# Performance work log

Hardware: AMD Instinct MI355X
Metric: run time of the kernel (lower is better)

The kernel has to match this reference:

```python
import jax, jax.numpy as jnp
import numpy as np


def setup_inputs() -> dict:
    key = jax.random.key(0)
    k0, k1 = jax.random.split(key)
    b, n, m, e = 8, 2048, 2048, 1024
    mat_0 = jax.random.normal(k0, (b, n, e), dtype=jnp.float32)
    mat_1 = jax.random.normal(k1, (b, m, e), dtype=jnp.float32)
    return {"mat_0": mat_0, "mat_1": mat_1}


def reference(mat_0, mat_1):
    # Original tiles to [b,n,m,e], multiplies, and sums over e.
    # Mathematically identical to a batched QK^T matmul: [b,n,m].
    return jnp.einsum('bne,bme->bnm', mat_0, mat_1)
```

## Files before the change

### kernel.cpp

```cpp
#include <hip/hip_runtime.h>
#include <hip/hip_bf16.h>

typedef __attribute__((ext_vector_type(8))) short short8;
typedef __attribute__((ext_vector_type(4))) float f32x4;
typedef __attribute__((ext_vector_type(4))) unsigned int u32x4;
typedef unsigned short u16;
typedef __attribute__((address_space(1))) void gvoid;
typedef __attribute__((address_space(3))) void lvoid;

static constexpr int BATCH = 8;
static constexpr int NDIM  = 2048;
static constexpr int MDIM  = 2048;
static constexpr int EDIM  = 1024;
static constexpr int BM    = 128;
static constexpr int BN    = 128;
static constexpr int BK    = 32;
static constexpr int KIT   = EDIM / BK;

__device__ __forceinline__ unsigned bf16rne_pair(float a, float b) {
  unsigned ua = __float_as_uint(a), ub = __float_as_uint(b);
  ua = (ua + 0x7FFFu + ((ua >> 16) & 1u)) >> 16;
  ub = (ub + 0x7FFFu + ((ub >> 16) & 1u)) >> 16;
  return ua | (ub << 16);
}

__global__ __launch_bounds__(256)
void cvt_kernel(const float* __restrict__ A, const float* __restrict__ B,
                u16* __restrict__ Abf, u16* __restrict__ Bbf) {
  const int half = (BATCH * NDIM * EDIM) / (256 * 8);
  int bid = blockIdx.x;
  const float* src; u16* dst;
  if (bid < half) { src = A; dst = Abf; }
  else            { src = B; dst = Bbf; bid -= half; }
  size_t idx = ((size_t)bid * 256 + threadIdx.x) * 8;
  f32x4 x = *(const f32x4*)(src + idx);
  f32x4 y = *(const f32x4*)(src + idx + 4);
  u32x4 r;
  r[0] = bf16rne_pair(x[0], x[1]);
  r[1] = bf16rne_pair(x[2], x[3]);
  r[2] = bf16rne_pair(y[0], y[1]);
  r[3] = bf16rne_pair(y[2], y[3]);
  *(u32x4*)(dst + idx) = r;
}

__device__ __forceinline__ void async_cp16(const void* g, void* l) {
  __builtin_amdgcn_global_load_lds((gvoid*)g, (lvoid*)l, 16, 0, 0);
}

__global__ __launch_bounds__(256, 3)
void bmm_bf16_kernel(const u16* __restrict__ A, const u16* __restrict__ B,
                     float* __restrict__ C) {
  __shared__ u16 As[BM * BK];
  __shared__ u16 Bs[BN * BK];

  const int tid  = threadIdx.x;
  const int lane = tid & 63;
  const int wave = tid >> 6;
  const int quad = lane >> 4;
  const int ml   = lane & 15;
  const int wrow = (wave >> 1) * 64;
  const int wcol = (wave & 1) * 64;

  const int tcol  = blockIdx.x;
  const int trow  = blockIdx.y;
  const int batch = blockIdx.z;

  const u16* Ab = A + (size_t)batch * NDIM * EDIM + (size_t)trow * BM * EDIM;
  const u16* Bb = B + (size_t)batch * MDIM * EDIM + (size_t)tcol * BN * EDIM;
  float*     Cb = C + (size_t)batch * NDIM * MDIM;

  const int rA0 = wave * 16;
  const int rA1 = wave * 16 + 64;
  const int lrow = lane >> 2;
  const int lcol = (lane & 3) * 8;

  const u16* gA0 = Ab + (size_t)(rA0 + lrow) * EDIM + lcol;
  const u16* gA1 = Ab + (size_t)(rA1 + lrow) * EDIM + lcol;
  const u16* gB0 = Bb + (size_t)(rA0 + lrow) * EDIM + lcol;
  const u16* gB1 = Bb + (size_t)(rA1 + lrow) * EDIM + lcol;
  u16* lA0 = &As[rA0 * BK];
  u16* lA1 = &As[rA1 * BK];
  u16* lB0 = &Bs[rA0 * BK];
  u16* lB1 = &Bs[rA1 * BK];

  f32x4 acc[4][4] = {};

  for (int kb = 0; kb < KIT; ++kb) {
    const int ko = kb * BK;
    __syncthreads();
    async_cp16(gA0 + ko, lA0);
    async_cp16(gA1 + ko, lA1);
    async_cp16(gB0 + ko, lB0);
    async_cp16(gB1 + ko, lB1);
    __syncthreads();

    short8 af[4], bfr[4];
#pragma unroll
    for (int i = 0; i < 4; ++i)
      af[i] = *(const short8*)&As[(wrow + i * 16 + ml) * BK + quad * 8];
#pragma unroll
    for (int i = 0; i < 4; ++i)
      bfr[i] = *(const short8*)&Bs[(wcol + i * 16 + ml) * BK + quad * 8];

#pragma unroll
    for (int mi = 0; mi < 4; ++mi)
#pragma unroll
      for (int ni = 0; ni < 4; ++ni)
        acc[mi][ni] = __builtin_amdgcn_mfma_f32_16x16x32_bf16(
            af[mi], bfr[ni], acc[mi][ni], 0, 0, 0);
  }

  const int crow = trow * BM + wrow + quad * 4;
  const int ccol = tcol * BN + wcol + ml;
#pragma unroll
  for (int mi = 0; mi < 4; ++mi) {
#pragma unroll
    for (int ni = 0; ni < 4; ++ni) {
      float* cp = Cb + (size_t)(crow + mi * 16) * MDIM + (ccol + ni * 16);
#pragma unroll
      for (int r = 0; r < 4; ++r)
        cp[(size_t)r * MDIM] = acc[mi][ni][r];
    }
  }
}

static constexpr int LSTR = 40;

__device__ __forceinline__ unsigned pk(float lo, float hi) {
  return __builtin_amdgcn_perm(__float_as_uint(hi), __float_as_uint(lo), 0x07060302u);
}
__device__ __forceinline__ u32x4 pack8(f32x4 x, f32x4 y) {
  u32x4 r;
  r[0] = pk(x[0], x[1]); r[1] = pk(x[2], x[3]);
  r[2] = pk(y[0], y[1]); r[3] = pk(y[2], y[3]);
  return r;
}

__global__ __launch_bounds__(256, 3)
void bmm_bt_kernel(const float* __restrict__ A, const float* __restrict__ B,
                   float* __restrict__ C) {
  __shared__ u16 As[BM * LSTR];
  __shared__ u16 Bs[BN * LSTR];

  const int tid  = threadIdx.x;
  const int lane = tid & 63;
  const int wave = tid >> 6;
  const int quad = lane >> 4;
  const int ml   = lane & 15;
  const int wrow = (wave >> 1) * 64;
  const int wcol = (wave & 1) * 64;

  const int tcol  = blockIdx.x;
  const int trow  = blockIdx.y;
  const int batch = blockIdx.z;

  const float* Ab = A + (size_t)batch * NDIM * EDIM + (size_t)trow * BM * EDIM;
  const float* Bb = B + (size_t)batch * MDIM * EDIM + (size_t)tcol * BN * EDIM;
  float*       Cb = C + (size_t)batch * NDIM * MDIM;

  const int r0 = tid >> 2;
  const int p0 = (tid & 3) * 8;
  const int r1 = r0 + 64;

  const float* pA0 = Ab + (size_t)r0 * EDIM + p0;
  const float* pA1 = Ab + (size_t)r1 * EDIM + p0;
  const float* pB0 = Bb + (size_t)r0 * EDIM + p0;
  const float* pB1 = Bb + (size_t)r1 * EDIM + p0;

  u16* wA0 = &As[r0 * LSTR + p0];
  u16* wA1 = &As[r1 * LSTR + p0];
  u16* wB0 = &Bs[r0 * LSTR + p0];
  u16* wB1 = &Bs[r1 * LSTR + p0];

  f32x4 a0 = *(const f32x4*)(pA0);
  f32x4 a1 = *(const f32x4*)(pA0 + 4);
  f32x4 a2 = *(const f32x4*)(pA1);
  f32x4 a3 = *(const f32x4*)(pA1 + 4);
  f32x4 b0 = *(const f32x4*)(pB0);
  f32x4 b1 = *(const f32x4*)(pB0 + 4);
  f32x4 b2 = *(const f32x4*)(pB1);
  f32x4 b3 = *(const f32x4*)(pB1 + 4);

  f32x4 acc[4][4] = {};

  for (int kb = 0; kb < KIT; ++kb) {
    __syncthreads();
    *(u32x4*)wA0 = pack8(a0, a1);
    *(u32x4*)wA1 = pack8(a2, a3);
    *(u32x4*)wB0 = pack8(b0, b1);
    *(u32x4*)wB1 = pack8(b2, b3);
    __syncthreads();

    if (kb + 1 < KIT) {
      const int off = (kb + 1) * BK;
      a0 = *(const f32x4*)(pA0 + off);
      a1 = *(const f32x4*)(pA0 + off + 4);
      a2 = *(const f32x4*)(pA1 + off);
      a3 = *(const f32x4*)(pA1 + off + 4);
      b0 = *(const f32x4*)(pB0 + off);
      b1 = *(const f32x4*)(pB0 + off + 4);
      b2 = *(const f32x4*)(pB1 + off);
      b3 = *(const f32x4*)(pB1 + off + 4);
    }

    short8 af[4], bfr[4];
#pragma unroll
    for (int i = 0; i < 4; ++i)
      af[i] = *(const short8*)&As[(wrow + i * 16 + ml) * LSTR + quad * 8];
#pragma unroll
    for (int i = 0; i < 4; ++i)
      bfr[i] = *(const short8*)&Bs[(wcol + i * 16 + ml) * LSTR + quad * 8];

#pragma unroll
    for (int mi = 0; mi < 4; ++mi)
#pragma unroll
      for (int ni = 0; ni < 4; ++ni)
        acc[mi][ni] = __builtin_amdgcn_mfma_f32_16x16x32_bf16(
            af[mi], bfr[ni], acc[mi][ni], 0, 0, 0);
  }

  const int crow = trow * BM + wrow + quad * 4;
  const int ccol = tcol * BN + wcol + ml;
#pragma unroll
  for (int mi = 0; mi < 4; ++mi) {
#pragma unroll
    for (int ni = 0; ni < 4; ++ni) {
      float* cp = Cb + (size_t)(crow + mi * 16) * MDIM + (ccol + ni * 16);
#pragma unroll
      for (int r = 0; r < 4; ++r)
        cp[(size_t)r * MDIM] = acc[mi][ni][r];
    }
  }
}

extern "C" void kernel_launch(void* const* d_in, const int* in_sizes, int n_in,
                              void* d_out, int out_size, void* d_ws, size_t ws_size,
                              hipStream_t stream) {
  const float* A = (const float*)d_in[0];
  const float* B = (const float*)d_in[1];
  float*       C = (float*)d_out;

  const size_t elems = (size_t)BATCH * NDIM * EDIM;
  const size_t need  = 2 * elems * sizeof(u16);

  if (ws_size >= need) {
    u16* Abf = (u16*)d_ws;
    u16* Bbf = Abf + elems;
    const int cvt_blocks = (int)(2 * elems / (256 * 8));
    cvt_kernel<<<cvt_blocks, 256, 0, stream>>>(A, B, Abf, Bbf);
    dim3 grid(MDIM / BN, NDIM / BM, BATCH);
    bmm_bf16_kernel<<<grid, dim3(256), 0, stream>>>(Abf, Bbf, C);
  } else {
    dim3 grid(MDIM / BN, NDIM / BM, BATCH);
    bmm_bt_kernel<<<grid, dim3(256), 0, stream>>>(A, B, C);
  }
}
```

Measured before the change: 303.3 us.

## Replace bf16 GEMM with 256x256 eight-phase pipelined kernel with double-buffered LDS

Replaces the 128x128x32 bf16 GEMM kernel with a 256x256x64 tile kernel using 512 threads (8 waves). Global-to-LDS async copies are double-buffered and interleaved with MFMA phases, ordered by explicit vmcnt waits and barriers. LDS is laid out with an XOR swizzle to avoid bank conflicts, and s_setprio is raised around the MFMA blocks. The aim is to hide load latency and raise arithmetic intensity, at the cost of 128 KB LDS per block, high register pressure, and fragile hand-coded wait counts.

```diff
diff --git a/kernel.cpp b/kernel.cpp
--- a/kernel.cpp
+++ b/kernel.cpp
@@ -12,10 +12,6 @@
 static constexpr int NDIM  = 2048;
 static constexpr int MDIM  = 2048;
 static constexpr int EDIM  = 1024;
-static constexpr int BM    = 128;
-static constexpr int BN    = 128;
-static constexpr int BK    = 32;
-static constexpr int KIT   = EDIM / BK;
 
 __device__ __forceinline__ unsigned bf16rne_pair(float a, float b) {
   unsigned ua = __float_as_uint(a), ub = __float_as_uint(b);
@@ -47,11 +43,181 @@
   __builtin_amdgcn_global_load_lds((gvoid*)g, (lvoid*)l, 16, 0, 0);
 }
 
+#define BAR() do { asm volatile("" ::: "memory"); \
+                   __builtin_amdgcn_s_barrier(); \
+                   asm volatile("" ::: "memory"); } while (0)
+#define WAITVM(N) asm volatile("s_waitcnt vmcnt(" #N ")" ::: "memory")
+
+static constexpr int BM = 256;
+static constexpr int BN = 256;
+static constexpr int BK = 64;
+static constexpr int KTILES = EDIM / BK;
+
+__global__ __launch_bounds__(512, 2)
+void bmm_8ph_kernel(const u16* __restrict__ A, const u16* __restrict__ B,
+                    float* __restrict__ C) {
+  __shared__ u16 sh[2][2][BM * BK];
+
+  const int tid  = threadIdx.x;
+  const int lane = tid & 63;
+  const int wave = tid >> 6;
+  const int wr   = wave >> 2;
+  const int wc   = wave & 3;
+  const int quad = lane >> 4;
+  const int ml   = lane & 15;
+
+  const int tcol  = blockIdx.x;
+  const int trow  = blockIdx.y;
+  const int batch = blockIdx.z;
+
+  const u16* Ab = A + (size_t)batch * NDIM * EDIM + (size_t)trow * BM * EDIM;
+  const u16* Bb = B + (size_t)batch * MDIM * EDIM + (size_t)tcol * BN * EDIM;
+
+  const int r0 = tid >> 3;
+  const int cs = (tid & 7) ^ (r0 & 7);
+  const u16* gA = Ab + (size_t)r0 * EDIM + cs * 8;
+  const u16* gB = Bb + (size_t)r0 * EDIM + cs * 8;
+
+#define STG(buf, ab, h, gptr, t) do {                                          \
+    const u16* _g = (gptr) + (size_t)((h) * 128) * EDIM + (size_t)(t) * BK;    \
+    async_cp16(_g,                   &sh[buf][ab][(h) * 8192 + wave * 512]);   \
+    async_cp16(_g + (size_t)64 * EDIM,                                         \
+               &sh[buf][ab][(h) * 8192 + 4096 + wave * 512]);                  \
+  } while (0)
+
+  const int aBase = (wr * 128 + ml) * 64;
+  const int bBase = (wc * 64 + ml) * 64;
+  const int kc0 = ((quad     ) ^ (ml & 7)) * 8;
+  const int kc1 = ((quad + 4 ) ^ (ml & 7)) * 8;
+
+  short8 ar[4][2], br0[2][2], br1[2][2];
+  f32x4 acc[8][4] = {};
+
+#define LDA(buf, mh) do {                                                      \
+    _Pragma("unroll")                                                          \
+    for (int q = 0; q < 4; ++q) {                                              \
+      ar[q][0] = *(const short8*)&sh[buf][0][aBase + (mh)*4096 + q*1024 + kc0];\
+      ar[q][1] = *(const short8*)&sh[buf][0][aBase + (mh)*4096 + q*1024 + kc1];\
+    } } while (0)
+
+#define LDB(dst, buf, nh) do {                                                 \
+    _Pragma("unroll")                                                          \
+    for (int n = 0; n < 2; ++n) {                                              \
+      dst[n][0] = *(const short8*)&sh[buf][1][bBase + (nh)*2048 + n*1024 + kc0];\
+      dst[n][1] = *(const short8*)&sh[buf][1][bBase + (nh)*2048 + n*1024 + kc1];\
+    } } while (0)
+
+#define MM(mh, nh, BSRC) do {                                                  \
+    __builtin_amdgcn_s_setprio(1);                                             \
+    _Pragma("unroll")                                                          \
+    for (int q = 0; q < 4; ++q)                                                \
+      _Pragma("unroll")                                                        \
+      for (int n = 0; n < 2; ++n)                                              \
+        _Pragma("unroll")                                                      \
+        for (int ks = 0; ks < 2; ++ks)                                         \
+          acc[(mh)*4 + q][(nh)*2 + n] = __builtin_amdgcn_mfma_f32_16x16x32_bf16(\
+              ar[q][ks], BSRC[n][ks], acc[(mh)*4 + q][(nh)*2 + n], 0, 0, 0);   \
+    __builtin_amdgcn_s_setprio(0);                                             \
+  } while (0)
+
+  STG(0, 0, 0, gA, 0);
+  STG(0, 0, 1, gA, 0);
+  STG(0, 1, 0, gB, 0);
+  STG(0, 1, 1, gB, 0);
+  STG(1, 1, 0, gB, 1);
+  STG(1, 1, 1, gB, 1);
+  WAITVM(4);
+  BAR();
+
+#pragma unroll 1
+  for (int i = 0; i < 7; ++i) {
+    const int t1 = 2 * i + 1, p0 = 2 * i + 2, p1 = 2 * i + 3;
+    LDA(0, 0); LDB(br0, 0, 0);
+    STG(1, 0, 0, gA, t1);
+    BAR(); MM(0, 0, br0); BAR();
+    LDB(br1, 0, 1);
+    STG(1, 0, 1, gA, t1);
+    BAR(); MM(0, 1, br1); BAR();
+    LDA(0, 1);
+    STG(0, 1, 0, gB, p0);
+    BAR(); MM(1, 1, br1); BAR();
+    STG(0, 1, 1, gB, p0);
+    WAITVM(4);
+    BAR(); MM(1, 0, br0); BAR();
+    LDA(1, 0); LDB(br0, 1, 0);
+    STG(0, 0, 0, gA, p0);
+    BAR(); MM(0, 0, br0); BAR();
+    LDB(br1, 1, 1);
+    STG(0, 0, 1, gA, p0);
+    BAR(); MM(0, 1, br1); BAR();
+    LDA(1, 1);
+    STG(1, 1, 0, gB, p1);
+    BAR(); MM(1, 1, br1); BAR();
+    STG(1, 1, 1, gB, p1);
+    WAITVM(4);
+    BAR(); MM(1, 0, br0); BAR();
+  }
+
+  {
+    LDA(0, 0); LDB(br0, 0, 0);
+    STG(1, 0, 0, gA, 15);
+    BAR(); MM(0, 0, br0); BAR();
+    LDB(br1, 0, 1);
+    STG(1, 0, 1, gA, 15);
+    BAR(); MM(0, 1, br1); BAR();
+    LDA(0, 1);
+    BAR(); MM(1, 1, br1); BAR();
+    WAITVM(0);
+    BAR(); MM(1, 0, br0); BAR();
+    LDA(1, 0); LDB(br0, 1, 0);
+    BAR(); MM(0, 0, br0); BAR();
+    LDB(br1, 1, 1);
+    BAR(); MM(0, 1, br1); BAR();
+    LDA(1, 1);
+    BAR(); MM(1, 1, br1); BAR();
+    MM(1, 0, br0);
+  }
+
+  float* Cb = C + (size_t)batch * NDIM * MDIM
+                + (size_t)(trow * BM + wr * 128 + quad * 4) * MDIM
+                + (tcol * BN + wc * 64 + ml);
+#pragma unroll
+  for (int mi = 0; mi < 8; ++mi) {
+#pragma unroll
+    for (int ni = 0; ni < 4; ++ni) {
+      float* cp = Cb + (size_t)(mi * 16) * MDIM + ni * 16;
+#pragma unroll
+      for (int r = 0; r < 4; ++r)
+        cp[(size_t)r * MDIM] = acc[mi][ni][r];
+    }
+  }
+#undef STG
+#undef LDA
+#undef LDB
+#undef MM
+}
+
+static constexpr int FBM = 128;
+static constexpr int FBN = 128;
+static constexpr int FBK = 32;
+static constexpr int FKIT = EDIM / FBK;
+static constexpr int LSTR = 40;
+
+__device__ __forceinline__ unsigned pk(float lo, float hi) {
+  return __builtin_amdgcn_perm(__float_as_uint(hi), __float_as_uint(lo), 0x07060302u);
+}
+__device__ __forceinline__ u32x4 pack8(f32x4 x, f32x4 y) {
+  u32x4 r;
+  r[0] = pk(x[0], x[1]); r[1] = pk(x[2], x[3]);
+  r[2] = pk(y[0], y[1]); r[3] = pk(y[2], y[3]);
+  return r;
+}
+
 __global__ __launch_bounds__(256, 3)
-void bmm_bf16_kernel(const u16* __restrict__ A, const u16* __restrict__ B,
-                     float* __restrict__ C) {
-  __shared__ u16 As[BM * BK];
-  __shared__ u16 Bs[BN * BK];
+void bmm_bt_kernel(const float* __restrict__ A, const float* __restrict__ B,
+                   float* __restrict__ C) {
+  __shared__ u16 As[FBM * LSTR];
+  __shared__ u16 Bs[FBN * LSTR];
 
   const int tid  = threadIdx.x;
   const int lane = tid & 63;
@@ -65,97 +231,8 @@
   const int trow  = blockIdx.y;
   const int batch = blockIdx.z;
 
-  const u16* Ab = A + (size_t)batch * NDIM * EDIM + (size_t)trow * BM * EDIM;
-  const u16* Bb = B + (size_t)batch * MDIM * EDIM + (size_t)tcol * BN * EDIM;
-  float*     Cb = C + (size_t)batch * NDIM * MDIM;
-
-  const int rA0 = wave * 16;
-  const int rA1 = wave * 16 + 64;
-  const int lrow = lane >> 2;
-  const int lcol = (lane & 3) * 8;
-
-  const u16* gA0 = Ab + (size_t)(rA0 + lrow) * EDIM + lcol;
-  const u16* gA1 = Ab + (size_t)(rA1 + lrow) * EDIM + lcol;
-  const u16* gB0 = Bb + (size_t)(rA0 + lrow) * EDIM + lcol;
-  const u16* gB1 = Bb + (size_t)(rA1 + lrow) * EDIM + lcol;
-  u16* lA0 = &As[rA0 * BK];
-  u16* lA1 = &As[rA1 * BK];
-  u16* lB0 = &Bs[rA0 * BK];
-  u16* lB1 = &Bs[rA1 * BK];
-
-  f32x4 acc[4][4] = {};
-
-  for (int kb = 0; kb < KIT; ++kb) {
-    const int ko = kb * BK;
-    __syncthreads();
-    async_cp16(gA0 + ko, lA0);
-    async_cp16(gA1 + ko, lA1);
-    async_cp16(gB0 + ko, lB0);
-    async_cp16(gB1 + ko, lB1);
-    __syncthreads();
-
-    short8 af[4], bfr[4];
-#pragma unroll
-    for (int i = 0; i < 4; ++i)
-      af[i] = *(const short8*)&As[(wrow + i * 16 + ml) * BK + quad * 8];
-#pragma unroll
-    for (int i = 0; i < 4; ++i)
-      bfr[i] = *(const short8*)&Bs[(wcol + i * 16 + ml) * BK + quad * 8];
-
-#pragma unroll
-    for (int mi = 0; mi < 4; ++mi)
-#pragma unroll
-      for (int ni = 0; ni < 4; ++ni)
-        acc[mi][ni] = __builtin_amdgcn_mfma_f32_16x16x32_bf16(
-            af[mi], bfr[ni], acc[mi][ni], 0, 0, 0);
-  }
-
-  const int crow = trow * BM + wrow + quad * 4;
-  const int ccol = tcol * BN + wcol + ml;
-#pragma unroll
-  for (int mi = 0; mi < 4; ++mi) {
-#pragma unroll
-    for (int ni = 0; ni < 4; ++ni) {
-      float* cp = Cb + (size_t)(crow + mi * 16) * MDIM + (ccol + ni * 16);
-#pragma unroll
-      for (int r = 0; r < 4; ++r)
-        cp[(size_t)r * MDIM] = acc[mi][ni][r];
-    }
-  }
-}
-
-static constexpr int LSTR = 40;
-
-__device__ __forceinline__ unsigned pk(float lo, float hi) {
-  return __builtin_amdgcn_perm(__float_as_uint(hi), __float_as_uint(lo), 0x07060302u);
-}
-__device__ __forceinline__ u32x4 pack8(f32x4 x, f32x4 y) {
-  u32x4 r;
-  r[0] = pk(x[0], x[1]); r[1] = pk(x[2], x[3]);
-  r[2] = pk(y[0], y[1]); r[3] = pk(y[2], y[3]);
-  return r;
-}
-
-__global__ __launch_bounds__(256, 3)
-void bmm_bt_kernel(const float* __restrict__ A, const float* __restrict__ B,
-                   float* __restrict__ C) {
-  __shared__ u16 As[BM * LSTR];
-  __shared__ u16 Bs[BN * LSTR];
-
-  const int tid  = threadIdx.x;
-  const int lane = tid & 63;
-  const int wave = tid >> 6;
-  const int quad = lane >> 4;
-  const int ml   = lane & 15;
-  const int wrow = (wave >> 1) * 64;
-  const int wcol = (wave & 1) * 64;
-
-  const int tcol  = blockIdx.x;
-  const int trow  = blockIdx.y;
-  const int batch = blockIdx.z;
-
-  const float* Ab = A + (size_t)batch * NDIM * EDIM + (size_t)trow * BM * EDIM;
-  const float* Bb = B + (size_t)batch * MDIM * EDIM + (size_t)tcol * BN * EDIM;
+  const float* Ab = A + (size_t)batch * NDIM * EDIM + (size_t)trow * FBM * EDIM;
+  const float* Bb = B + (size_t)batch * MDIM * EDIM + (size_t)tcol * FBN * EDIM;
   float*       Cb = C + (size_t)batch * NDIM * MDIM;
 
   const int r0 = tid >> 2;
@@ -183,7 +260,7 @@
 
   f32x4 acc[4][4] = {};
 
-  for (int kb = 0; kb < KIT; ++kb) {
+  for (int kb = 0; kb < FKIT; ++kb) {
     __syncthreads();
     *(u32x4*)wA0 = pack8(a0, a1);
     *(u32x4*)wA1 = pack8(a2, a3);
@@ -191,8 +268,8 @@
     *(u32x4*)wB1 = pack8(b2, b3);
     __syncthreads();
 
-    if (kb + 1 < KIT) {
-      const int off = (kb + 1) * BK;
+    if (kb + 1 < FKIT) {
+      const int off = (kb + 1) * FBK;
       a0 = *(const f32x4*)(pA0 + off);
       a1 = *(const f32x4*)(pA0 + off + 4);
       a2 = *(const f32x4*)(pA1 + off);
@@ -219,8 +296,8 @@
             af[mi], bfr[ni], acc[mi][ni], 0, 0, 0);
   }
 
-  const int crow = trow * BM + wrow + quad * 4;
-  const int ccol = tcol * BN + wcol + ml;
+  const int crow = trow * FBM + wrow + quad * 4;
+  const int ccol = tcol * FBN + wcol + ml;
 #pragma unroll
   for (int mi = 0; mi < 4; ++mi) {
 #pragma unroll
@@ -249,9 +326,9 @@
     const int cvt_blocks = (int)(2 * elems / (256 * 8));
     cvt_kernel<<<cvt_blocks, 256, 0, stream>>>(A, B, Abf, Bbf);
     dim3 grid(MDIM / BN, NDIM / BM, BATCH);
-    bmm_bf16_kernel<<<grid, dim3(256), 0, stream>>>(Abf, Bbf, C);
+    bmm_8ph_kernel<<<grid, dim3(512), 0, stream>>>(Abf, Bbf, C);
   } else {
-    dim3 grid(MDIM / BN, NDIM / BM, BATCH);
+    dim3 grid(MDIM / FBN, NDIM / FBM, BATCH);
     bmm_bt_kernel<<<grid, dim3(256), 0, stream>>>(A, B, C);
   }
 }
```

After: 288.9 us. -4.8%, faster.
